# Performance work log

Measured on AMD Instinct MI355X. Metric: run time of the kernel, lower is better.

## Reference

```python
import jax, jax.numpy as jnp
import numpy as np

N = 131072      # total nodes
B = 512         # number of graphs
F_DIM = 512     # in_channels
H = F_DIM // 2  # score_net hidden
RATIO = 0.5
MARGIN = 0.5
TOPK_LOSS_WEIGHT = 0.2


def setup_inputs() -> dict:
    key = jax.random.key(0)
    k1, k2, k3 = jax.random.split(key, 3)
    x = jax.random.normal(k1, (N, F_DIM), dtype=jnp.float32)
    # sorted segment ids: equal-sized graphs of N // B nodes
    batch = (jnp.arange(N) // (N // B)).astype(jnp.int32)
    W1 = jax.random.normal(k2, (F_DIM, H), dtype=jnp.float32) / np.sqrt(F_DIM).astype(np.float32)
    b1 = jnp.zeros((H,), dtype=jnp.float32)
    W2 = jax.random.normal(k3, (H, 1), dtype=jnp.float32) / np.sqrt(H).astype(np.float32)
    b2 = jnp.zeros((1,), dtype=jnp.float32)
    return {"x": x, "batch": batch, "W1": W1, "b1": b1, "W2": W2, "b2": b2}


def reference(x, batch, W1, b1, W2, b2):
    # scores = score_net(x).squeeze(-1)   [N]
    scores = (jax.nn.relu(x @ W1 + b1) @ W2 + b2)[:, 0]

    # per-graph node counts and k = max(1, int(ratio * n_i))
    counts = jax.ops.segment_sum(jnp.ones((N,), dtype=scores.dtype), batch, num_segments=B)
    k = jnp.maximum(1, jnp.floor(RATIO * counts).astype(jnp.int32))  # [B]

    # segmented top-k via lexsort: sort by (batch asc, score desc)
    order = jnp.lexsort((-scores, batch))          # [N] permutation
    b_sorted = batch[order]
    starts = jnp.cumsum(counts) - counts           # exclusive-cumsum segment starts
    rank = jnp.arange(N, dtype=counts.dtype) - starts[b_sorted]  # rank within graph (0 = highest score)
    sel_sorted = rank < k[b_sorted].astype(counts.dtype)
    selected_mask = jnp.zeros((N,), dtype=bool).at[order].set(sel_sorted)

    # global_add_pool over selected nodes
    m = selected_mask.astype(x.dtype)
    x_pooled = jax.ops.segment_sum(x * m[:, None], batch, num_segments=B)  # [B, F]

    # margin regularization loss per graph
    sel_cnt = jax.ops.segment_sum(m, batch, num_segments=B)
    sel_sum = jax.ops.segment_sum(scores * m, batch, num_segments=B)
    tot_sum = jax.ops.segment_sum(scores, batch, num_segments=B)
    uns_cnt = counts - sel_cnt
    sel_mean = sel_sum / jnp.maximum(sel_cnt, 1.0)
    uns_mean = (tot_sum - sel_sum) / jnp.maximum(uns_cnt, 1.0)
    per_graph = jnp.where(uns_cnt > 0, jax.nn.relu(MARGIN - (sel_mean - uns_mean)), 0.0)
    topk_loss = per_graph.sum() / B * TOPK_LOSS_WEIGHT

    return x_pooled, topk_loss, selected_mask
```

## Files before the change

### kernel.cpp

```cpp
#include <hip/hip_runtime.h>

#define N_NODES 131072
#define BGRAPHS 512
#define FDIM    512
#define HDIM    256
#define NPG     256
#define KSEL    128
#define STAGES  16
#define BSTAGE_SHORTS 24576
#define A_ROW   40
#define A_PLANE (NPG * A_ROW)

typedef __attribute__((ext_vector_type(8)))  short bf16x8;
typedef __attribute__((ext_vector_type(16))) float f32x16;

__device__ __forceinline__ unsigned short bf16_rne(float f, float* back) {
    unsigned u = __float_as_uint(f);
    unsigned r = u + 0x7FFFu + ((u >> 16) & 1u);
    unsigned short h = (unsigned short)(r >> 16);
    *back = __uint_as_float(((unsigned)h) << 16);
    return h;
}

__global__ __launch_bounds__(256)
void split_w1_kernel(const float* __restrict__ W1, unsigned short* __restrict__ wsB)
{
    const int uid  = blockIdx.x * 256 + threadIdx.x;
    const int lane = uid & 63;
    int t = uid >> 6;
    const int nt = t & 7;  t >>= 3;
    const int p  = t % 3;  t /= 3;
    const int q  = t & 1;
    const int s  = t >> 1;
    const int n  = nt * 32 + (lane & 31);
    const int k0 = s * 32 + q * 16 + (lane >> 5) * 8;

    bf16x8 v;
    #pragma unroll
    for (int j = 0; j < 8; ++j) {
        float w = W1[(size_t)(k0 + j) * HDIM + n];
        float f1, f2, f3;
        unsigned short h1 = bf16_rne(w, &f1);
        float r1 = w - f1;
        unsigned short h2 = bf16_rne(r1, &f2);
        float r2 = r1 - f2;
        unsigned short h3 = bf16_rne(r2, &f3);
        v[j] = (short)(p == 0 ? h1 : (p == 1 ? h2 : h3));
    }
    *(bf16x8*)(wsB + (size_t)uid * 8) = v;
}

__global__ __launch_bounds__(512, 2)
void fused_kernel(const float* __restrict__ x,
                  const unsigned short* __restrict__ wsB,
                  const float* __restrict__ b1, const float* __restrict__ W2,
                  const float* __restrict__ b2,
                  float* __restrict__ pooled, float* __restrict__ mask_out,
                  float* __restrict__ loss_per_g)
{
    __shared__ __attribute__((aligned(16))) unsigned char smem[2 * 49152 + 3 * A_PLANE * 2];
    unsigned short* ldsA = (unsigned short*)(smem + 2 * 49152);

    const int g    = blockIdx.x;
    const int tid  = threadIdx.x;
    const int lane = tid & 63;
    const int wv   = tid >> 6;
    const int wy   = wv & 3;
    const int wx   = wv >> 2;
    const int l31  = lane & 31;
    const int lh   = lane >> 5;

    const int r  = tid >> 1;
    const int hf = tid & 1;
    const float* aptr = x + ((size_t)(g * NPG + r)) * FDIM + hf * 16;

    f32x16 acc[2][4];
    #pragma unroll
    for (int a = 0; a < 2; ++a)
        #pragma unroll
        for (int b = 0; b < 4; ++b)
            #pragma unroll
            for (int rr = 0; rr < 16; ++rr) acc[a][b][rr] = 0.f;

    float4 pf0, pf1, pf2, pf3;

    pf0 = *(const float4*)(aptr + 0);
    pf1 = *(const float4*)(aptr + 4);
    pf2 = *(const float4*)(aptr + 8);
    pf3 = *(const float4*)(aptr + 12);
    {
        const unsigned short* src = wsB;
        #pragma unroll
        for (int i = 0; i < 6; ++i) {
            const int unit = i * 512 + tid;
            __builtin_amdgcn_global_load_lds(
                (const __attribute__((address_space(1))) unsigned int*)(src + (size_t)unit * 8),
                (__attribute__((address_space(3))) unsigned int*)((unsigned short*)smem + unit * 8),
                16, 0, 0);
        }
    }
    {
        float v[16] = {pf0.x, pf0.y, pf0.z, pf0.w, pf1.x, pf1.y, pf1.z, pf1.w,
                       pf2.x, pf2.y, pf2.z, pf2.w, pf3.x, pf3.y, pf3.z, pf3.w};
        unsigned short H[16], M[16], L[16];
        #pragma unroll
        for (int j = 0; j < 16; ++j) {
            float f1, f2, f3;
            H[j] = bf16_rne(v[j], &f1);
            float r1 = v[j] - f1;
            M[j] = bf16_rne(r1, &f2);
            float r2 = r1 - f2;
            L[j] = bf16_rne(r2, &f3);
        }
        const int base = r * A_ROW + hf * 16;
        const unsigned short* P[3] = {H, M, L};
        #pragma unroll
        for (int p = 0; p < 3; ++p) {
            const unsigned short* s8 = P[p];
            uint4 u0, u1;
            u0.x = (unsigned)s8[0] | ((unsigned)s8[1] << 16);
            u0.y = (unsigned)s8[2] | ((unsigned)s8[3] << 16);
            u0.z = (unsigned)s8[4] | ((unsigned)s8[5] << 16);
            u0.w = (unsigned)s8[6] | ((unsigned)s8[7] << 16);
            u1.x = (unsigned)s8[8] | ((unsigned)s8[9] << 16);
            u1.y = (unsigned)s8[10] | ((unsigned)s8[11] << 16);
            u1.z = (unsigned)s8[12] | ((unsigned)s8[13] << 16);
            u1.w = (unsigned)s8[14] | ((unsigned)s8[15] << 16);
            uint4* dst = (uint4*)(ldsA + p * A_PLANE + base);
            dst[0] = u0;
            dst[1] = u1;
        }
    }
    __syncthreads();

    for (int s = 0; s < STAGES; ++s) {
        if (s < STAGES - 1) {
            const unsigned short* src = wsB + (size_t)(s + 1) * BSTAGE_SHORTS;
            unsigned short* dstB = (unsigned short*)smem + ((s + 1) & 1) * BSTAGE_SHORTS;
            #pragma unroll
            for (int i = 0; i < 6; ++i) {
                const int unit = i * 512 + tid;
                __builtin_amdgcn_global_load_lds(
                    (const __attribute__((address_space(1))) unsigned int*)(src + (size_t)unit * 8),
                    (__attribute__((address_space(3))) unsigned int*)(dstB + unit * 8),
                    16, 0, 0);
            }
            const float* ap = aptr + (s + 1) * 32;
            pf0 = *(const float4*)(ap + 0);
            pf1 = *(const float4*)(ap + 4);
            pf2 = *(const float4*)(ap + 8);
            pf3 = *(const float4*)(ap + 12);
        }

        const bf16x8* bfp = (const bf16x8*)((unsigned short*)smem + (s & 1) * BSTAGE_SHORTS);
        #pragma unroll
        for (int q = 0; q < 2; ++q) {
            bf16x8 Bh[4], Bm[4], Bl[4];
            #pragma unroll
            for (int nt = 0; nt < 4; ++nt) {
                const int nn = wx * 4 + nt;
                Bh[nt] = bfp[((q * 3 + 0) * 8 + nn) * 64 + lane];
                Bm[nt] = bfp[((q * 3 + 1) * 8 + nn) * 64 + lane];
                Bl[nt] = bfp[((q * 3 + 2) * 8 + nn) * 64 + lane];
            }
            #pragma unroll
            for (int mt = 0; mt < 2; ++mt) {
                const int m = wy * 64 + mt * 32 + l31;
                const int aoff = m * A_ROW + q * 16 + lh * 8;
                bf16x8 Ah = *(const bf16x8*)(ldsA + 0 * A_PLANE + aoff);
                bf16x8 Am = *(const bf16x8*)(ldsA + 1 * A_PLANE + aoff);
                bf16x8 Al = *(const bf16x8*)(ldsA + 2 * A_PLANE + aoff);
                #pragma unroll
                for (int nt = 0; nt < 4; ++nt) {
                    acc[mt][nt] = __builtin_amdgcn_mfma_f32_32x32x16_bf16(Ah, Bh[nt], acc[mt][nt], 0, 0, 0);
                    acc[mt][nt] = __builtin_amdgcn_mfma_f32_32x32x16_bf16(Ah, Bm[nt], acc[mt][nt], 0, 0, 0);
                    acc[mt][nt] = __builtin_amdgcn_mfma_f32_32x32x16_bf16(Am, Bh[nt], acc[mt][nt], 0, 0, 0);
                    acc[mt][nt] = __builtin_amdgcn_mfma_f32_32x32x16_bf16(Ah, Bl[nt], acc[mt][nt], 0, 0, 0);
                    acc[mt][nt] = __builtin_amdgcn_mfma_f32_32x32x16_bf16(Al, Bh[nt], acc[mt][nt], 0, 0, 0);
                    acc[mt][nt] = __builtin_amdgcn_mfma_f32_32x32x16_bf16(Am, Bm[nt], acc[mt][nt], 0, 0, 0);
                }
            }
        }
        __syncthreads();

        if (s < STAGES - 1) {
            float v[16] = {pf0.x, pf0.y, pf0.z, pf0.w, pf1.x, pf1.y, pf1.z, pf1.w,
                           pf2.x, pf2.y, pf2.z, pf2.w, pf3.x, pf3.y, pf3.z, pf3.w};
            unsigned short H[16], M[16], L[16];
            #pragma unroll
            for (int j = 0; j < 16; ++j) {
                float f1, f2, f3;
                H[j] = bf16_rne(v[j], &f1);
                float r1 = v[j] - f1;
                M[j] = bf16_rne(r1, &f2);
                float r2 = r1 - f2;
                L[j] = bf16_rne(r2, &f3);
            }
            const int base = r * A_ROW + hf * 16;
            const unsigned short* P[3] = {H, M, L};
            #pragma unroll
            for (int p = 0; p < 3; ++p) {
                const unsigned short* s8 = P[p];
                uint4 u0, u1;
                u0.x = (unsigned)s8[0] | ((unsigned)s8[1] << 16);
                u0.y = (unsigned)s8[2] | ((unsigned)s8[3] << 16);
                u0.z = (unsigned)s8[4] | ((unsigned)s8[5] << 16);
                u0.w = (unsigned)s8[6] | ((unsigned)s8[7] << 16);
                u1.x = (unsigned)s8[8] | ((unsigned)s8[9] << 16);
                u1.y = (unsigned)s8[10] | ((unsigned)s8[11] << 16);
                u1.z = (unsigned)s8[12] | ((unsigned)s8[13] << 16);
                u1.w = (unsigned)s8[14] | ((unsigned)s8[15] << 16);
                uint4* dst = (uint4*)(ldsA + p * A_PLANE + base);
                dst[0] = u0;
                dst[1] = u1;
            }
        }
        __syncthreads();
    }

    float* Sp   = (float*)smem;
    float* sv   = Sp + 2 * NPG;
    int*   selr = (int*)(sv + NPG);
    float* redT = (float*)(selr + KSEL);
    float* redS = redT + NPG;

    float bb[4], ww[4];
    #pragma unroll
    for (int nt = 0; nt < 4; ++nt) {
        const int c = wx * 128 + nt * 32 + l31;
        bb[nt] = b1[c];
        ww[nt] = W2[c];
    }
    #pragma unroll
    for (int mt = 0; mt < 2; ++mt) {
        float pr[16];
        #pragma unroll
        for (int rr = 0; rr < 16; ++rr) pr[rr] = 0.f;
        #pragma unroll
        for (int nt = 0; nt < 4; ++nt)
            #pragma unroll
            for (int rr = 0; rr < 16; ++rr) {
                float h = acc[mt][nt][rr] + bb[nt];
                h = h > 0.f ? h : 0.f;
                pr[rr] = fmaf(h, ww[nt], pr[rr]);
            }
        #pragma unroll
        for (int mask = 1; mask <= 16; mask <<= 1)
            #pragma unroll
            for (int rr = 0; rr < 16; ++rr)
                pr[rr] += __shfl_xor(pr[rr], mask);
        if (l31 == 0) {
            #pragma unroll
            for (int rr = 0; rr < 16; ++rr) {
                const int row = wy * 64 + mt * 32 + (rr & 3) + 8 * (rr >> 2) + 4 * lh;
                Sp[wx * NPG + row] = pr[rr];
            }
        }
    }
    __syncthreads();

    float sc = 0.f;
    if (tid < NPG) {
        sc = b2[0] + Sp[tid] + Sp[NPG + tid];
        sv[tid] = sc;
    }
    __syncthreads();

    if (tid < NPG) {
        int rank = 0;
        for (int j = 0; j < NPG; ++j) {
            const float sj = sv[j];
            rank += (sj > sc || (sj == sc && j < tid)) ? 1 : 0;
        }
        const bool sel = rank < KSEL;
        mask_out[g * NPG + tid] = sel ? 1.0f : 0.0f;
        if (sel) selr[rank] = tid;
        redT[tid] = sc;
        redS[tid] = sel ? sc : 0.f;
    }
    __syncthreads();

    for (int off = 128; off > 0; off >>= 1) {
        if (tid < off) { redT[tid] += redT[tid + off]; redS[tid] += redS[tid + off]; }
        __syncthreads();
    }
    if (tid == 0) {
        const float tot = redT[0], ssum = redS[0];
        const float sel_mean = ssum * (1.0f / KSEL);
        const float uns_mean = (tot - ssum) * (1.0f / (NPG - KSEL));
        const float v = 0.5f - (sel_mean - uns_mean);
        loss_per_g[g] = v > 0.f ? v : 0.f;
    }

    const int col = tid;
    const float* __restrict__ xg = x + (size_t)g * NPG * FDIM;
    float a0 = 0.f, a1 = 0.f, a2 = 0.f, a3 = 0.f;
    #pragma unroll 4
    for (int n = 0; n < KSEL; n += 4) {
        a0 += xg[(size_t)selr[n + 0] * FDIM + col];
        a1 += xg[(size_t)selr[n + 1] * FDIM + col];
        a2 += xg[(size_t)selr[n + 2] * FDIM + col];
        a3 += xg[(size_t)selr[n + 3] * FDIM + col];
    }
    pooled[g * FDIM + col] = (a0 + a1) + (a2 + a3);
}

__global__ __launch_bounds__(256)
void loss_kernel(const float* __restrict__ loss_per_g, float* __restrict__ out_loss)
{
    __shared__ float red[256];
    const int t = threadIdx.x;
    red[t] = loss_per_g[t] + loss_per_g[t + 256];
    __syncthreads();
    for (int off = 128; off > 0; off >>= 1) {
        if (t < off) red[t] += red[t + off];
        __syncthreads();
    }
    if (t == 0) out_loss[0] = red[0] * (0.2f / BGRAPHS);
}

extern "C" void kernel_launch(void* const* d_in, const int* in_sizes, int n_in,
                              void* d_out, int out_size, void* d_ws, size_t ws_size,
                              hipStream_t stream)
{
    const float* x  = (const float*)d_in[0];
    const float* W1 = (const float*)d_in[2];
    const float* b1 = (const float*)d_in[3];
    const float* W2 = (const float*)d_in[4];
    const float* b2 = (const float*)d_in[5];

    float* out    = (float*)d_out;
    float* pooled = out;
    float* loss   = out + BGRAPHS * FDIM;
    float* mask   = loss + 1;

    float* loss_g       = (float*)d_ws;
    unsigned short* wsB = (unsigned short*)((char*)d_ws + 4096);

    split_w1_kernel<<<192, 256, 0, stream>>>(W1, wsB);
    fused_kernel<<<BGRAPHS, 512, 0, stream>>>(x, wsB, b1, W2, b2,
                                              pooled, mask, loss_g);
    loss_kernel<<<1, 256, 0, stream>>>(loss_g, loss);
}
```

Before: 474.5 us.

## Double fused kernel block to 1024 threads, halving per-wave MFMA tile

Raises the fused kernel to 1024 threads per block (16 waves), so each wave computes a 64x64 output tile with 2x2 accumulators instead of 2x4. The x prefetch, B staging loads and the final pooling gather are split across twice as many threads, and the partial score and pool sums are combined through shared memory. The aim is more waves per block to hide memory latency and lower register pressure per wave. In exchange, each B fragment is reused across fewer A tiles, and the LDS traffic per MFMA and the synchronisation cost both grow.

```diff
diff --git a/kernel.cpp b/kernel.cpp
--- a/kernel.cpp
+++ b/kernel.cpp
@@ -50,7 +50,7 @@
     *(bf16x8*)(wsB + (size_t)uid * 8) = v;
 }
 
-__global__ __launch_bounds__(512, 2)
+__global__ __launch_bounds__(1024)
 void fused_kernel(const float* __restrict__ x,
                   const unsigned short* __restrict__ wsB,
                   const float* __restrict__ b1, const float* __restrict__ W2,
@@ -70,29 +70,27 @@
     const int l31  = lane & 31;
     const int lh   = lane >> 5;
 
-    const int r  = tid >> 1;
-    const int hf = tid & 1;
-    const float* aptr = x + ((size_t)(g * NPG + r)) * FDIM + hf * 16;
-
-    f32x16 acc[2][4];
+    const int r  = tid >> 2;
+    const int qf = tid & 3;
+    const float* aptr = x + ((size_t)(g * NPG + r)) * FDIM + qf * 8;
+
+    f32x16 acc[2][2];
     #pragma unroll
     for (int a = 0; a < 2; ++a)
         #pragma unroll
-        for (int b = 0; b < 4; ++b)
+        for (int b = 0; b < 2; ++b)
             #pragma unroll
             for (int rr = 0; rr < 16; ++rr) acc[a][b][rr] = 0.f;
 
-    float4 pf0, pf1, pf2, pf3;
+    float4 pf0, pf1;
 
     pf0 = *(const float4*)(aptr + 0);
     pf1 = *(const float4*)(aptr + 4);
-    pf2 = *(const float4*)(aptr + 8);
-    pf3 = *(const float4*)(aptr + 12);
     {
         const unsigned short* src = wsB;
         #pragma unroll
-        for (int i = 0; i < 6; ++i) {
-            const int unit = i * 512 + tid;
+        for (int i = 0; i < 3; ++i) {
+            const int unit = i * 1024 + tid;
             __builtin_amdgcn_global_load_lds(
                 (const __attribute__((address_space(1))) unsigned int*)(src + (size_t)unit * 8),
                 (__attribute__((address_space(3))) unsigned int*)((unsigned short*)smem + unit * 8),
@@ -100,11 +98,10 @@
         }
     }
     {
-        float v[16] = {pf0.x, pf0.y, pf0.z, pf0.w, pf1.x, pf1.y, pf1.z, pf1.w,
-                       pf2.x, pf2.y, pf2.z, pf2.w, pf3.x, pf3.y, pf3.z, pf3.w};
-        unsigned short H[16], M[16], L[16];
-        #pragma unroll
-        for (int j = 0; j < 16; ++j) {
+        float v[8] = {pf0.x, pf0.y, pf0.z, pf0.w, pf1.x, pf1.y, pf1.z, pf1.w};
+        unsigned short H[8], M[8], L[8];
+        #pragma unroll
+        for (int j = 0; j < 8; ++j) {
             float f1, f2, f3;
             H[j] = bf16_rne(v[j], &f1);
             float r1 = v[j] - f1;
@@ -112,23 +109,17 @@
             float r2 = r1 - f2;
             L[j] = bf16_rne(r2, &f3);
         }
-        const int base = r * A_ROW + hf * 16;
+        const int base = r * A_ROW + qf * 8;
         const unsigned short* P[3] = {H, M, L};
         #pragma unroll
         for (int p = 0; p < 3; ++p) {
             const unsigned short* s8 = P[p];
-            uint4 u0, u1;
-            u0.x = (unsigned)s8[0] | ((unsigned)s8[1] << 16);
-            u0.y = (unsigned)s8[2] | ((unsigned)s8[3] << 16);
-            u0.z = (unsigned)s8[4] | ((unsigned)s8[5] << 16);
-            u0.w = (unsigned)s8[6] | ((unsigned)s8[7] << 16);
-            u1.x = (unsigned)s8[8] | ((unsigned)s8[9] << 16);
-            u1.y = (unsigned)s8[10] | ((unsigned)s8[11] << 16);
-            u1.z = (unsigned)s8[12] | ((unsigned)s8[13] << 16);
-            u1.w = (unsigned)s8[14] | ((unsigned)s8[15] << 16);
-            uint4* dst = (uint4*)(ldsA + p * A_PLANE + base);
-            dst[0] = u0;
-            dst[1] = u1;
+            uint4 u;
+            u.x = (unsigned)s8[0] | ((unsigned)s8[1] << 16);
+            u.y = (unsigned)s8[2] | ((unsigned)s8[3] << 16);
+            u.z = (unsigned)s8[4] | ((unsigned)s8[5] << 16);
+            u.w = (unsigned)s8[6] | ((unsigned)s8[7] << 16);
+            *(uint4*)(ldsA + p * A_PLANE + base) = u;
         }
     }
     __syncthreads();
@@ -138,8 +129,8 @@
             const unsigned short* src = wsB + (size_t)(s + 1) * BSTAGE_SHORTS;
             unsigned short* dstB = (unsigned short*)smem + ((s + 1) & 1) * BSTAGE_SHORTS;
             #pragma unroll
-            for (int i = 0; i < 6; ++i) {
-                const int unit = i * 512 + tid;
+            for (int i = 0; i < 3; ++i) {
+                const int unit = i * 1024 + tid;
                 __builtin_amdgcn_global_load_lds(
                     (const __attribute__((address_space(1))) unsigned int*)(src + (size_t)unit * 8),
                     (__attribute__((address_space(3))) unsigned int*)(dstB + unit * 8),
@@ -148,47 +139,58 @@
             const float* ap = aptr + (s + 1) * 32;
             pf0 = *(const float4*)(ap + 0);
             pf1 = *(const float4*)(ap + 4);
-            pf2 = *(const float4*)(ap + 8);
-            pf3 = *(const float4*)(ap + 12);
         }
 
         const bf16x8* bfp = (const bf16x8*)((unsigned short*)smem + (s & 1) * BSTAGE_SHORTS);
         #pragma unroll
         for (int q = 0; q < 2; ++q) {
-            bf16x8 Bh[4], Bm[4], Bl[4];
-            #pragma unroll
-            for (int nt = 0; nt < 4; ++nt) {
-                const int nn = wx * 4 + nt;
-                Bh[nt] = bfp[((q * 3 + 0) * 8 + nn) * 64 + lane];
-                Bm[nt] = bfp[((q * 3 + 1) * 8 + nn) * 64 + lane];
-                Bl[nt] = bfp[((q * 3 + 2) * 8 + nn) * 64 + lane];
-            }
-            #pragma unroll
-            for (int mt = 0; mt < 2; ++mt) {
-                const int m = wy * 64 + mt * 32 + l31;
-                const int aoff = m * A_ROW + q * 16 + lh * 8;
-                bf16x8 Ah = *(const bf16x8*)(ldsA + 0 * A_PLANE + aoff);
-                bf16x8 Am = *(const bf16x8*)(ldsA + 1 * A_PLANE + aoff);
-                bf16x8 Al = *(const bf16x8*)(ldsA + 2 * A_PLANE + aoff);
-                #pragma unroll
-                for (int nt = 0; nt < 4; ++nt) {
-                    acc[mt][nt] = __builtin_amdgcn_mfma_f32_32x32x16_bf16(Ah, Bh[nt], acc[mt][nt], 0, 0, 0);
-                    acc[mt][nt] = __builtin_amdgcn_mfma_f32_32x32x16_bf16(Ah, Bm[nt], acc[mt][nt], 0, 0, 0);
-                    acc[mt][nt] = __builtin_amdgcn_mfma_f32_32x32x16_bf16(Am, Bh[nt], acc[mt][nt], 0, 0, 0);
-                    acc[mt][nt] = __builtin_amdgcn_mfma_f32_32x32x16_bf16(Ah, Bl[nt], acc[mt][nt], 0, 0, 0);
-                    acc[mt][nt] = __builtin_amdgcn_mfma_f32_32x32x16_bf16(Al, Bh[nt], acc[mt][nt], 0, 0, 0);
-                    acc[mt][nt] = __builtin_amdgcn_mfma_f32_32x32x16_bf16(Am, Bm[nt], acc[mt][nt], 0, 0, 0);
-                }
-            }
+            const int a0off = (wy * 64 + l31) * A_ROW + q * 16 + lh * 8;
+            const int a1off = a0off + 32 * A_ROW;
+            bf16x8 A0h = *(const bf16x8*)(ldsA + 0 * A_PLANE + a0off);
+            bf16x8 A0m = *(const bf16x8*)(ldsA + 1 * A_PLANE + a0off);
+            bf16x8 A0l = *(const bf16x8*)(ldsA + 2 * A_PLANE + a0off);
+            bf16x8 A1h = *(const bf16x8*)(ldsA + 0 * A_PLANE + a1off);
+            bf16x8 A1m = *(const bf16x8*)(ldsA + 1 * A_PLANE + a1off);
+            bf16x8 A1l = *(const bf16x8*)(ldsA + 2 * A_PLANE + a1off);
+            const int nb = wx * 2;
+            bf16x8 Bh0 = bfp[((q * 3 + 0) * 8 + nb + 0) * 64 + lane];
+            bf16x8 Bh1 = bfp[((q * 3 + 0) * 8 + nb + 1) * 64 + lane];
+            acc[0][0] = __builtin_amdgcn_mfma_f32_32x32x16_bf16(A0h, Bh0, acc[0][0], 0, 0, 0);
+            acc[0][1] = __builtin_amdgcn_mfma_f32_32x32x16_bf16(A0h, Bh1, acc[0][1], 0, 0, 0);
+            acc[1][0] = __builtin_amdgcn_mfma_f32_32x32x16_bf16(A1h, Bh0, acc[1][0], 0, 0, 0);
+            acc[1][1] = __builtin_amdgcn_mfma_f32_32x32x16_bf16(A1h, Bh1, acc[1][1], 0, 0, 0);
+            acc[0][0] = __builtin_amdgcn_mfma_f32_32x32x16_bf16(A0m, Bh0, acc[0][0], 0, 0, 0);
+            acc[0][1] = __builtin_amdgcn_mfma_f32_32x32x16_bf16(A0m, Bh1, acc[0][1], 0, 0, 0);
+            acc[1][0] = __builtin_amdgcn_mfma_f32_32x32x16_bf16(A1m, Bh0, acc[1][0], 0, 0, 0);
+            acc[1][1] = __builtin_amdgcn_mfma_f32_32x32x16_bf16(A1m, Bh1, acc[1][1], 0, 0, 0);
+            acc[0][0] = __builtin_amdgcn_mfma_f32_32x32x16_bf16(A0l, Bh0, acc[0][0], 0, 0, 0);
+            acc[0][1] = __builtin_amdgcn_mfma_f32_32x32x16_bf16(A0l, Bh1, acc[0][1], 0, 0, 0);
+            acc[1][0] = __builtin_amdgcn_mfma_f32_32x32x16_bf16(A1l, Bh0, acc[1][0], 0, 0, 0);
+            acc[1][1] = __builtin_amdgcn_mfma_f32_32x32x16_bf16(A1l, Bh1, acc[1][1], 0, 0, 0);
+            bf16x8 Bm0 = bfp[((q * 3 + 1) * 8 + nb + 0) * 64 + lane];
+            bf16x8 Bm1 = bfp[((q * 3 + 1) * 8 + nb + 1) * 64 + lane];
+            acc[0][0] = __builtin_amdgcn_mfma_f32_32x32x16_bf16(A0h, Bm0, acc[0][0], 0, 0, 0);
+            acc[0][1] = __builtin_amdgcn_mfma_f32_32x32x16_bf16(A0h, Bm1, acc[0][1], 0, 0, 0);
+            acc[1][0] = __builtin_amdgcn_mfma_f32_32x32x16_bf16(A1h, Bm0, acc[1][0], 0, 0, 0);
+            acc[1][1] = __builtin_amdgcn_mfma_f32_32x32x16_bf16(A1h, Bm1, acc[1][1], 0, 0, 0);
+            acc[0][0] = __builtin_amdgcn_mfma_f32_32x32x16_bf16(A0m, Bm0, acc[0][0], 0, 0, 0);
+            acc[0][1] = __builtin_amdgcn_mfma_f32_32x32x16_bf16(A0m, Bm1, acc[0][1], 0, 0, 0);
+            acc[1][0] = __builtin_amdgcn_mfma_f32_32x32x16_bf16(A1m, Bm0, acc[1][0], 0, 0, 0);
+            acc[1][1] = __builtin_amdgcn_mfma_f32_32x32x16_bf16(A1m, Bm1, acc[1][1], 0, 0, 0);
+            bf16x8 Bl0 = bfp[((q * 3 + 2) * 8 + nb + 0) * 64 + lane];
+            bf16x8 Bl1 = bfp[((q * 3 + 2) * 8 + nb + 1) * 64 + lane];
+            acc[0][0] = __builtin_amdgcn_mfma_f32_32x32x16_bf16(A0h, Bl0, acc[0][0], 0, 0, 0);
+            acc[0][1] = __builtin_amdgcn_mfma_f32_32x32x16_bf16(A0h, Bl1, acc[0][1], 0, 0, 0);
+            acc[1][0] = __builtin_amdgcn_mfma_f32_32x32x16_bf16(A1h, Bl0, acc[1][0], 0, 0, 0);
+            acc[1][1] = __builtin_amdgcn_mfma_f32_32x32x16_bf16(A1h, Bl1, acc[1][1], 0, 0, 0);
         }
         __syncthreads();
 
         if (s < STAGES - 1) {
-            float v[16] = {pf0.x, pf0.y, pf0.z, pf0.w, pf1.x, pf1.y, pf1.z, pf1.w,
-                           pf2.x, pf2.y, pf2.z, pf2.w, pf3.x, pf3.y, pf3.z, pf3.w};
-            unsigned short H[16], M[16], L[16];
-            #pragma unroll
-            for (int j = 0; j < 16; ++j) {
+            float v[8] = {pf0.x, pf0.y, pf0.z, pf0.w, pf1.x, pf1.y, pf1.z, pf1.w};
+            unsigned short H[8], M[8], L[8];
+            #pragma unroll
+            for (int j = 0; j < 8; ++j) {
                 float f1, f2, f3;
                 H[j] = bf16_rne(v[j], &f1);
                 float r1 = v[j] - f1;
@@ -196,38 +198,33 @@
                 float r2 = r1 - f2;
                 L[j] = bf16_rne(r2, &f3);
             }
-            const int base = r * A_ROW + hf * 16;
+            const int base = r * A_ROW + qf * 8;
             const unsigned short* P[3] = {H, M, L};
             #pragma unroll
             for (int p = 0; p < 3; ++p) {
                 const unsigned short* s8 = P[p];
-                uint4 u0, u1;
-                u0.x = (unsigned)s8[0] | ((unsigned)s8[1] << 16);
-                u0.y = (unsigned)s8[2] | ((unsigned)s8[3] << 16);
-                u0.z = (unsigned)s8[4] | ((unsigned)s8[5] << 16);
-                u0.w = (unsigned)s8[6] | ((unsigned)s8[7] << 16);
-                u1.x = (unsigned)s8[8] | ((unsigned)s8[9] << 16);
-                u1.y = (unsigned)s8[10] | ((unsigned)s8[11] << 16);
-                u1.z = (unsigned)s8[12] | ((unsigned)s8[13] << 16);
-                u1.w = (unsigned)s8[14] | ((unsigned)s8[15] << 16);
-                uint4* dst = (uint4*)(ldsA + p * A_PLANE + base);
-                dst[0] = u0;
-                dst[1] = u1;
+                uint4 u;
+                u.x = (unsigned)s8[0] | ((unsigned)s8[1] << 16);
+                u.y = (unsigned)s8[2] | ((unsigned)s8[3] << 16);
+                u.z = (unsigned)s8[4] | ((unsigned)s8[5] << 16);
+                u.w = (unsigned)s8[6] | ((unsigned)s8[7] << 16);
+                *(uint4*)(ldsA + p * A_PLANE + base) = u;
             }
         }
         __syncthreads();
     }
 
     float* Sp   = (float*)smem;
-    float* sv   = Sp + 2 * NPG;
+    float* sv   = Sp + 4 * NPG;
     int*   selr = (int*)(sv + NPG);
     float* redT = (float*)(selr + KSEL);
     float* redS = redT + NPG;
-
-    float bb[4], ww[4];
+    float* gprt = redS + NPG;
+
+    float bb[2], ww[2];
     #pragma unroll
-    for (int nt = 0; nt < 4; ++nt) {
-        const int c = wx * 128 + nt * 32 + l31;
+    for (int nt = 0; nt < 2; ++nt) {
+        const int c = wx * 64 + nt * 32 + l31;
         bb[nt] = b1[c];
         ww[nt] = W2[c];
     }
@@ -237,7 +234,7 @@
         #pragma unroll
         for (int rr = 0; rr < 16; ++rr) pr[rr] = 0.f;
         #pragma unroll
-        for (int nt = 0; nt < 4; ++nt)
+        for (int nt = 0; nt < 2; ++nt)
             #pragma unroll
             for (int rr = 0; rr < 16; ++rr) {
                 float h = acc[mt][nt][rr] + bb[nt];
@@ -261,7 +258,7 @@
 
     float sc = 0.f;
     if (tid < NPG) {
-        sc = b2[0] + Sp[tid] + Sp[NPG + tid];
+        sc = b2[0] + Sp[tid] + Sp[NPG + tid] + Sp[2 * NPG + tid] + Sp[3 * NPG + tid];
         sv[tid] = sc;
     }
     __syncthreads();
@@ -292,17 +289,22 @@
         loss_per_g[g] = v > 0.f ? v : 0.f;
     }
 
-    const int col = tid;
+    const int col = tid & 511;
+    const int h2  = tid >> 9;
     const float* __restrict__ xg = x + (size_t)g * NPG * FDIM;
     float a0 = 0.f, a1 = 0.f, a2 = 0.f, a3 = 0.f;
     #pragma unroll 4
-    for (int n = 0; n < KSEL; n += 4) {
-        a0 += xg[(size_t)selr[n + 0] * FDIM + col];
-        a1 += xg[(size_t)selr[n + 1] * FDIM + col];
-        a2 += xg[(size_t)selr[n + 2] * FDIM + col];
-        a3 += xg[(size_t)selr[n + 3] * FDIM + col];
-    }
-    pooled[g * FDIM + col] = (a0 + a1) + (a2 + a3);
+    for (int n = 0; n < 64; n += 4) {
+        const int base = h2 * 64 + n;
+        a0 += xg[(size_t)selr[base + 0] * FDIM + col];
+        a1 += xg[(size_t)selr[base + 1] * FDIM + col];
+        a2 += xg[(size_t)selr[base + 2] * FDIM + col];
+        a3 += xg[(size_t)selr[base + 3] * FDIM + col];
+    }
+    const float part = (a0 + a1) + (a2 + a3);
+    if (h2) gprt[col] = part;
+    __syncthreads();
+    if (!h2) pooled[g * FDIM + col] = part + gprt[col];
 }
 
 __global__ __launch_bounds__(256)
@@ -338,7 +340,7 @@
     unsigned short* wsB = (unsigned short*)((char*)d_ws + 4096);
 
     split_w1_kernel<<<192, 256, 0, stream>>>(W1, wsB);
-    fused_kernel<<<BGRAPHS, 512, 0, stream>>>(x, wsB, b1, W2, b2,
-                                              pooled, mask, loss_g);
+    fused_kernel<<<BGRAPHS, 1024, 0, stream>>>(x, wsB, b1, W2, b2,
+                                               pooled, mask, loss_g);
     loss_kernel<<<1, 256, 0, stream>>>(loss_g, loss);
 }
```

Measured after the change: 489.0 us. +3.1%, slower.

## Switch GEMM emulation from bf16x3 to scaled fp16x2 and double-buffer A tile

Applied to the files above, without the earlier changes.

Replaces the three-way bf16 split of x and W1 with a two-way fp16 split using power-of-two scaling, reducing MFMAs per tile from six to four (all hi/lo cross terms) and shrinking the staged B and A buffers. The A operand is now double-buffered in LDS with a two-stage unrolled loop so conversion of the next tile overlaps compute. Accumulators are unscaled in the epilogue. This risks fp16 range overflow or underflow for inputs outside the expected magnitude and uses more LDS for the extra A buffer.

```diff
diff --git a/kernel.cpp b/kernel.cpp
--- a/kernel.cpp
+++ b/kernel.cpp
@@ -1,25 +1,24 @@
 #include <hip/hip_runtime.h>
 
-#define N_NODES 131072
 #define BGRAPHS 512
 #define FDIM    512
 #define HDIM    256
 #define NPG     256
 #define KSEL    128
 #define STAGES  16
-#define BSTAGE_SHORTS 24576
+#define BSTAGE_SHORTS 16384
 #define A_ROW   40
 #define A_PLANE (NPG * A_ROW)
 
-typedef __attribute__((ext_vector_type(8)))  short bf16x8;
-typedef __attribute__((ext_vector_type(16))) float f32x16;
-
-__device__ __forceinline__ unsigned short bf16_rne(float f, float* back) {
-    unsigned u = __float_as_uint(f);
-    unsigned r = u + 0x7FFFu + ((u >> 16) & 1u);
-    unsigned short h = (unsigned short)(r >> 16);
-    *back = __uint_as_float(((unsigned)h) << 16);
-    return h;
+typedef __attribute__((ext_vector_type(8)))  _Float16 f16x8;
+typedef __attribute__((ext_vector_type(8)))  short    s16x8;
+typedef __attribute__((ext_vector_type(16))) float    f32x16;
+
+__device__ __forceinline__ unsigned short f16_rne(float f, float* back) {
+    _Float16 h = (_Float16)f;
+    *back = (float)h;
+    union { _Float16 h; unsigned short s; } cv; cv.h = h;
+    return cv.s;
 }
 
 __global__ __launch_bounds__(256)
@@ -29,25 +28,22 @@
     const int lane = uid & 63;
     int t = uid >> 6;
     const int nt = t & 7;  t >>= 3;
-    const int p  = t % 3;  t /= 3;
+    const int p  = t & 1;  t >>= 1;
     const int q  = t & 1;
     const int s  = t >> 1;
     const int n  = nt * 32 + (lane & 31);
     const int k0 = s * 32 + q * 16 + (lane >> 5) * 8;
 
-    bf16x8 v;
+    s16x8 v;
     #pragma unroll
     for (int j = 0; j < 8; ++j) {
-        float w = W1[(size_t)(k0 + j) * HDIM + n];
-        float f1, f2, f3;
-        unsigned short h1 = bf16_rne(w, &f1);
-        float r1 = w - f1;
-        unsigned short h2 = bf16_rne(r1, &f2);
-        float r2 = r1 - f2;
-        unsigned short h3 = bf16_rne(r2, &f3);
-        v[j] = (short)(p == 0 ? h1 : (p == 1 ? h2 : h3));
-    }
-    *(bf16x8*)(wsB + (size_t)uid * 8) = v;
+        float w = W1[(size_t)(k0 + j) * HDIM + n] * 1024.0f;
+        float f1, f2;
+        unsigned short h1 = f16_rne(w, &f1);
+        unsigned short h2 = f16_rne(w - f1, &f2);
+        v[j] = (short)(p ? h2 : h1);
+    }
+    *(s16x8*)(wsB + (size_t)uid * 8) = v;
 }
 
 __global__ __launch_bounds__(512, 2)
@@ -58,8 +54,7 @@
                   float* __restrict__ pooled, float* __restrict__ mask_out,
                   float* __restrict__ loss_per_g)
 {
-    __shared__ __attribute__((aligned(16))) unsigned char smem[2 * 49152 + 3 * A_PLANE * 2];
-    unsigned short* ldsA = (unsigned short*)(smem + 2 * 49152);
+    __shared__ __attribute__((aligned(16))) unsigned char smem[147456];
 
     const int g    = blockIdx.x;
     const int tid  = threadIdx.x;
@@ -82,139 +77,105 @@
             #pragma unroll
             for (int rr = 0; rr < 16; ++rr) acc[a][b][rr] = 0.f;
 
-    float4 pf0, pf1, pf2, pf3;
-
-    pf0 = *(const float4*)(aptr + 0);
-    pf1 = *(const float4*)(aptr + 4);
-    pf2 = *(const float4*)(aptr + 8);
-    pf3 = *(const float4*)(aptr + 12);
-    {
-        const unsigned short* src = wsB;
-        #pragma unroll
-        for (int i = 0; i < 6; ++i) {
-            const int unit = i * 512 + tid;
-            __builtin_amdgcn_global_load_lds(
-                (const __attribute__((address_space(1))) unsigned int*)(src + (size_t)unit * 8),
-                (__attribute__((address_space(3))) unsigned int*)((unsigned short*)smem + unit * 8),
-                16, 0, 0);
-        }
-    }
-    {
-        float v[16] = {pf0.x, pf0.y, pf0.z, pf0.w, pf1.x, pf1.y, pf1.z, pf1.w,
-                       pf2.x, pf2.y, pf2.z, pf2.w, pf3.x, pf3.y, pf3.z, pf3.w};
-        unsigned short H[16], M[16], L[16];
-        #pragma unroll
-        for (int j = 0; j < 16; ++j) {
-            float f1, f2, f3;
-            H[j] = bf16_rne(v[j], &f1);
-            float r1 = v[j] - f1;
-            M[j] = bf16_rne(r1, &f2);
-            float r2 = r1 - f2;
-            L[j] = bf16_rne(r2, &f3);
-        }
-        const int base = r * A_ROW + hf * 16;
-        const unsigned short* P[3] = {H, M, L};
-        #pragma unroll
-        for (int p = 0; p < 3; ++p) {
-            const unsigned short* s8 = P[p];
-            uint4 u0, u1;
-            u0.x = (unsigned)s8[0] | ((unsigned)s8[1] << 16);
-            u0.y = (unsigned)s8[2] | ((unsigned)s8[3] << 16);
-            u0.z = (unsigned)s8[4] | ((unsigned)s8[5] << 16);
-            u0.w = (unsigned)s8[6] | ((unsigned)s8[7] << 16);
-            u1.x = (unsigned)s8[8] | ((unsigned)s8[9] << 16);
-            u1.y = (unsigned)s8[10] | ((unsigned)s8[11] << 16);
-            u1.z = (unsigned)s8[12] | ((unsigned)s8[13] << 16);
-            u1.w = (unsigned)s8[14] | ((unsigned)s8[15] << 16);
-            uint4* dst = (uint4*)(ldsA + p * A_PLANE + base);
-            dst[0] = u0;
-            dst[1] = u1;
-        }
-    }
-    __syncthreads();
-
-    for (int s = 0; s < STAGES; ++s) {
-        if (s < STAGES - 1) {
-            const unsigned short* src = wsB + (size_t)(s + 1) * BSTAGE_SHORTS;
-            unsigned short* dstB = (unsigned short*)smem + ((s + 1) & 1) * BSTAGE_SHORTS;
-            #pragma unroll
-            for (int i = 0; i < 6; ++i) {
-                const int unit = i * 512 + tid;
-                __builtin_amdgcn_global_load_lds(
-                    (const __attribute__((address_space(1))) unsigned int*)(src + (size_t)unit * 8),
-                    (__attribute__((address_space(3))) unsigned int*)(dstB + unit * 8),
-                    16, 0, 0);
-            }
-            const float* ap = aptr + (s + 1) * 32;
-            pf0 = *(const float4*)(ap + 0);
-            pf1 = *(const float4*)(ap + 4);
-            pf2 = *(const float4*)(ap + 8);
-            pf3 = *(const float4*)(ap + 12);
-        }
-
-        const bf16x8* bfp = (const bf16x8*)((unsigned short*)smem + (s & 1) * BSTAGE_SHORTS);
-        #pragma unroll
-        for (int q = 0; q < 2; ++q) {
-            bf16x8 Bh[4], Bm[4], Bl[4];
-            #pragma unroll
-            for (int nt = 0; nt < 4; ++nt) {
-                const int nn = wx * 4 + nt;
-                Bh[nt] = bfp[((q * 3 + 0) * 8 + nn) * 64 + lane];
-                Bm[nt] = bfp[((q * 3 + 1) * 8 + nn) * 64 + lane];
-                Bl[nt] = bfp[((q * 3 + 2) * 8 + nn) * 64 + lane];
-            }
-            #pragma unroll
-            for (int mt = 0; mt < 2; ++mt) {
-                const int m = wy * 64 + mt * 32 + l31;
-                const int aoff = m * A_ROW + q * 16 + lh * 8;
-                bf16x8 Ah = *(const bf16x8*)(ldsA + 0 * A_PLANE + aoff);
-                bf16x8 Am = *(const bf16x8*)(ldsA + 1 * A_PLANE + aoff);
-                bf16x8 Al = *(const bf16x8*)(ldsA + 2 * A_PLANE + aoff);
-                #pragma unroll
-                for (int nt = 0; nt < 4; ++nt) {
-                    acc[mt][nt] = __builtin_amdgcn_mfma_f32_32x32x16_bf16(Ah, Bh[nt], acc[mt][nt], 0, 0, 0);
-                    acc[mt][nt] = __builtin_amdgcn_mfma_f32_32x32x16_bf16(Ah, Bm[nt], acc[mt][nt], 0, 0, 0);
-                    acc[mt][nt] = __builtin_amdgcn_mfma_f32_32x32x16_bf16(Am, Bh[nt], acc[mt][nt], 0, 0, 0);
-                    acc[mt][nt] = __builtin_amdgcn_mfma_f32_32x32x16_bf16(Ah, Bl[nt], acc[mt][nt], 0, 0, 0);
-                    acc[mt][nt] = __builtin_amdgcn_mfma_f32_32x32x16_bf16(Al, Bh[nt], acc[mt][nt], 0, 0, 0);
-                    acc[mt][nt] = __builtin_amdgcn_mfma_f32_32x32x16_bf16(Am, Bm[nt], acc[mt][nt], 0, 0, 0);
-                }
-            }
-        }
+    float4 aA0, aA1, aA2, aA3;
+    float4 aB0, aB1, aB2, aB3;
+
+#define GLL_B(S1) do {                                                          \
+    const unsigned short* _src = wsB + (size_t)(S1) * BSTAGE_SHORTS;            \
+    unsigned short* _dst = (unsigned short*)smem + ((S1) & 1) * BSTAGE_SHORTS;  \
+    _Pragma("unroll")                                                           \
+    for (int _i = 0; _i < 4; ++_i) {                                            \
+        const int _u = _i * 512 + tid;                                          \
+        __builtin_amdgcn_global_load_lds(                                       \
+            (const __attribute__((address_space(1))) unsigned int*)(_src + (size_t)_u * 8), \
+            (__attribute__((address_space(3))) unsigned int*)(_dst + _u * 8),   \
+            16, 0, 0);                                                          \
+    } } while (0)
+
+#define LOAD_PF(P0,P1,P2,P3,S2) do {                                            \
+    const float* _ap = aptr + (S2) * 32;                                        \
+    P0 = *(const float4*)(_ap + 0);  P1 = *(const float4*)(_ap + 4);            \
+    P2 = *(const float4*)(_ap + 8);  P3 = *(const float4*)(_ap + 12); } while (0)
+
+#define CONVERT_A(P0,P1,P2,P3,BUF) do {                                         \
+    float _v[16] = {P0.x,P0.y,P0.z,P0.w,P1.x,P1.y,P1.z,P1.w,                    \
+                    P2.x,P2.y,P2.z,P2.w,P3.x,P3.y,P3.z,P3.w};                   \
+    unsigned short _H[16], _M[16];                                              \
+    _Pragma("unroll")                                                           \
+    for (int _j = 0; _j < 16; ++_j) {                                           \
+        float _f1, _f2;                                                         \
+        float _xs = _v[_j] * 64.0f;                            \
+        _H[_j] = f16_rne(_xs, &_f1);                                            \
+        _M[_j] = f16_rne(_xs - _f1, &_f2);                                      \
+        (void)_f2;                                                              \
+    }                                                                           \
+    unsigned short* _pl = (unsigned short*)(smem + 65536 + (BUF) * 40960)       \
+                          + r * A_ROW + hf * 16;                                \
+    uint4 _u0, _u1;                                                             \
+    _u0.x = (unsigned)_H[0]  | ((unsigned)_H[1]  << 16);                        \
+    _u0.y = (unsigned)_H[2]  | ((unsigned)_H[3]  << 16);                        \
+    _u0.z = (unsigned)_H[4]  | ((unsigned)_H[5]  << 16);                        \
+    _u0.w = (unsigned)_H[6]  | ((unsigned)_H[7]  << 16);                        \
+    _u1.x = (unsigned)_H[8]  | ((unsigned)_H[9]  << 16);                        \
+    _u1.y = (unsigned)_H[10] | ((unsigned)_H[11] << 16);                        \
+    _u1.z = (unsigned)_H[12] | ((unsigned)_H[13] << 16);                        \
+    _u1.w = (unsigned)_H[14] | ((unsigned)_H[15] << 16);                        \
+    ((uint4*)_pl)[0] = _u0; ((uint4*)_pl)[1] = _u1;                             \
+    _u0.x = (unsigned)_M[0]  | ((unsigned)_M[1]  << 16);                        \
+    _u0.y = (unsigned)_M[2]  | ((unsigned)_M[3]  << 16);                        \
+    _u0.z = (unsigned)_M[4]  | ((unsigned)_M[5]  << 16);                        \
+    _u0.w = (unsigned)_M[6]  | ((unsigned)_M[7]  << 16);                        \
+    _u1.x = (unsigned)_M[8]  | ((unsigned)_M[9]  << 16);                        \
+    _u1.y = (unsigned)_M[10] | ((unsigned)_M[11] << 16);                        \
+    _u1.z = (unsigned)_M[12] | ((unsigned)_M[13] << 16);                        \
+    _u1.w = (unsigned)_M[14] | ((unsigned)_M[15] << 16);                        \
+    ((uint4*)(_pl + A_PLANE))[0] = _u0; ((uint4*)(_pl + A_PLANE))[1] = _u1;     \
+    } while (0)
+
+#define COMPUTE(BUF) do {                                                       \
+    const f16x8* _bfp = (const f16x8*)(smem + (BUF) * (BSTAGE_SHORTS * 2));     \
+    const unsigned short* _aB = (const unsigned short*)(smem + 65536 + (BUF) * 40960); \
+    _Pragma("unroll")                                                           \
+    for (int _q = 0; _q < 2; ++_q) {                                            \
+        const int _a0 = (wy * 64 + l31) * A_ROW + _q * 16 + lh * 8;             \
+        const int _a1 = _a0 + 32 * A_ROW;                                       \
+        f16x8 A0h = *(const f16x8*)(_aB + _a0);                                 \
+        f16x8 A0m = *(const f16x8*)(_aB + A_PLANE + _a0);                       \
+        f16x8 A1h = *(const f16x8*)(_aB + _a1);                                 \
+        f16x8 A1m = *(const f16x8*)(_aB + A_PLANE + _a1);                       \
+        _Pragma("unroll")                                                       \
+        for (int _nt = 0; _nt < 4; ++_nt) {                                     \
+            const int _nn = wx * 4 + _nt;                                       \
+            f16x8 Bh = _bfp[((_q * 2 + 0) * 8 + _nn) * 64 + lane];              \
+            f16x8 Bm = _bfp[((_q * 2 + 1) * 8 + _nn) * 64 + lane];              \
+            acc[0][_nt] = __builtin_amdgcn_mfma_f32_32x32x16_f16(A0h, Bh, acc[0][_nt], 0, 0, 0); \
+            acc[1][_nt] = __builtin_amdgcn_mfma_f32_32x32x16_f16(A1h, Bh, acc[1][_nt], 0, 0, 0); \
+            acc[0][_nt] = __builtin_amdgcn_mfma_f32_32x32x16_f16(A0m, Bh, acc[0][_nt], 0, 0, 0); \
+            acc[1][_nt] = __builtin_amdgcn_mfma_f32_32x32x16_f16(A1m, Bh, acc[1][_nt], 0, 0, 0); \
+            acc[0][_nt] = __builtin_amdgcn_mfma_f32_32x32x16_f16(A0h, Bm, acc[0][_nt], 0, 0, 0); \
+            acc[1][_nt] = __builtin_amdgcn_mfma_f32_32x32x16_f16(A1h, Bm, acc[1][_nt], 0, 0, 0); \
+            acc[0][_nt] = __builtin_amdgcn_mfma_f32_32x32x16_f16(A0m, Bm, acc[0][_nt], 0, 0, 0); \
+            acc[1][_nt] = __builtin_amdgcn_mfma_f32_32x32x16_f16(A1m, Bm, acc[1][_nt], 0, 0, 0); \
+        }                                                                       \
+    } } while (0)
+
+    LOAD_PF(aA0, aA1, aA2, aA3, 0);
+    GLL_B(0);
+    CONVERT_A(aA0, aA1, aA2, aA3, 0);
+    LOAD_PF(aA0, aA1, aA2, aA3, 1);
+    __syncthreads();
+
+    for (int s = 0; s < STAGES; s += 2) {
+        if (s < STAGES - 1) GLL_B(s + 1);
+        if (s < STAGES - 2) LOAD_PF(aB0, aB1, aB2, aB3, s + 2);
+        COMPUTE(0);
+        if (s < STAGES - 1) CONVERT_A(aA0, aA1, aA2, aA3, 1);
         __syncthreads();
 
-        if (s < STAGES - 1) {
-            float v[16] = {pf0.x, pf0.y, pf0.z, pf0.w, pf1.x, pf1.y, pf1.z, pf1.w,
-                           pf2.x, pf2.y, pf2.z, pf2.w, pf3.x, pf3.y, pf3.z, pf3.w};
-            unsigned short H[16], M[16], L[16];
-            #pragma unroll
-            for (int j = 0; j < 16; ++j) {
-                float f1, f2, f3;
-                H[j] = bf16_rne(v[j], &f1);
-                float r1 = v[j] - f1;
-                M[j] = bf16_rne(r1, &f2);
-                float r2 = r1 - f2;
-                L[j] = bf16_rne(r2, &f3);
-            }
-            const int base = r * A_ROW + hf * 16;
-            const unsigned short* P[3] = {H, M, L};
-            #pragma unroll
-            for (int p = 0; p < 3; ++p) {
-                const unsigned short* s8 = P[p];
-                uint4 u0, u1;
-                u0.x = (unsigned)s8[0] | ((unsigned)s8[1] << 16);
-                u0.y = (unsigned)s8[2] | ((unsigned)s8[3] << 16);
-                u0.z = (unsigned)s8[4] | ((unsigned)s8[5] << 16);
-                u0.w = (unsigned)s8[6] | ((unsigned)s8[7] << 16);
-                u1.x = (unsigned)s8[8] | ((unsigned)s8[9] << 16);
-                u1.y = (unsigned)s8[10] | ((unsigned)s8[11] << 16);
-                u1.z = (unsigned)s8[12] | ((unsigned)s8[13] << 16);
-                u1.w = (unsigned)s8[14] | ((unsigned)s8[15] << 16);
-                uint4* dst = (uint4*)(ldsA + p * A_PLANE + base);
-                dst[0] = u0;
-                dst[1] = u1;
-            }
-        }
+        if (s + 1 < STAGES - 1) GLL_B(s + 2);
+        if (s + 1 < STAGES - 2) LOAD_PF(aA0, aA1, aA2, aA3, s + 3);
+        COMPUTE(1);
+        if (s + 1 < STAGES - 1) CONVERT_A(aB0, aB1, aB2, aB3, 0);
         __syncthreads();
     }
 
@@ -231,6 +192,7 @@
         bb[nt] = b1[c];
         ww[nt] = W2[c];
     }
+    const float unscale = 1.0f / 65536.0f;
     #pragma unroll
     for (int mt = 0; mt < 2; ++mt) {
         float pr[16];
@@ -240,7 +202,7 @@
         for (int nt = 0; nt < 4; ++nt)
             #pragma unroll
             for (int rr = 0; rr < 16; ++rr) {
-                float h = acc[mt][nt][rr] + bb[nt];
+                float h = fmaf(acc[mt][nt][rr], unscale, bb[nt]);
                 h = h > 0.f ? h : 0.f;
                 pr[rr] = fmaf(h, ww[nt], pr[rr]);
             }
@@ -303,6 +265,11 @@
         a3 += xg[(size_t)selr[n + 3] * FDIM + col];
     }
     pooled[g * FDIM + col] = (a0 + a1) + (a2 + a3);
+
+#undef GLL_B
+#undef LOAD_PF
+#undef CONVERT_A
+#undef COMPUTE
 }
 
 __global__ __launch_bounds__(256)
@@ -337,7 +304,7 @@
     float* loss_g       = (float*)d_ws;
     unsigned short* wsB = (unsigned short*)((char*)d_ws + 4096);
 
-    split_w1_kernel<<<192, 256, 0, stream>>>(W1, wsB);
+    split_w1_kernel<<<128, 256, 0, stream>>>(W1, wsB);
     fused_kernel<<<BGRAPHS, 512, 0, stream>>>(x, wsB, b1, W2, b2,
                                               pooled, mask, loss_g);
     loss_kernel<<<1, 256, 0, stream>>>(loss_g, loss);
```

New measurement: 434.3 us. 1.09x faster.
